# Performance work log

Measured on AMD Instinct MI355X. Metric: run time of the kernel, lower is better.

The kernel has to match this reference:

```python
import jax, jax.numpy as jnp
import numpy as np

B, S, D = 4, 2048, 768   # batch, seq_len, dim_inp
H, E = 12, 64            # num_heads, dim_out (per-head)
LN_EPS = 1e-5


def setup_inputs() -> dict:
    key = jax.random.key(0)
    ks = jax.random.split(key, 12)
    sd = 1.0 / np.sqrt(D)
    x = jax.random.normal(ks[0], (B, S, D), dtype=jnp.float32)
    Wq = jax.random.normal(ks[1], (H, D, E), dtype=jnp.float32) * sd
    bq = jax.random.normal(ks[2], (H, E), dtype=jnp.float32) * 0.02
    Wk = jax.random.normal(ks[3], (H, D, E), dtype=jnp.float32) * sd
    bk = jax.random.normal(ks[4], (H, E), dtype=jnp.float32) * 0.02
    Wv = jax.random.normal(ks[5], (H, D, E), dtype=jnp.float32) * sd
    bv = jax.random.normal(ks[6], (H, E), dtype=jnp.float32) * 0.02
    Wo = jax.random.normal(ks[7], (H * E, D), dtype=jnp.float32) * (1.0 / np.sqrt(H * E))
    bo = jax.random.normal(ks[8], (D,), dtype=jnp.float32) * 0.02
    gamma = jnp.ones((D,), dtype=jnp.float32)
    beta = jnp.zeros((D,), dtype=jnp.float32)
    return {"input_tensor": x, "Wq": Wq, "bq": bq, "Wk": Wk, "bk": bk,
            "Wv": Wv, "bv": bv, "Wo": Wo, "bo": bo, "gamma": gamma, "beta": beta}


def reference(input_tensor, Wq, bq, Wk, bk, Wv, bv, Wo, bo, gamma, beta):
    x = input_tensor  # [B,S,D]
    # all heads at once: [B,H,S,E]
    q = jnp.einsum('bsd,hde->bhse', x, Wq) + bq[None, :, None, :]
    k = jnp.einsum('bsd,hde->bhse', x, Wk) + bk[None, :, None, :]
    v = jnp.einsum('bsd,hde->bhse', x, Wv) + bv[None, :, None, :]
    # NOTE: original divides by sqrt(seq_len) (query.size(1)), not sqrt(head_dim)
    scale = jnp.sqrt(jnp.float32(q.shape[2]))
    scores = jnp.einsum('bhse,bhte->bhst', q, k) / scale  # [B,H,S,S]
    attn = jax.nn.softmax(scores, axis=-1)
    ctx = jnp.einsum('bhst,bhte->bhse', attn, v)          # [B,H,S,E]
    # concat heads along last dim: [B,S,H*E]
    ctx = ctx.transpose(0, 2, 1, 3).reshape(x.shape[0], x.shape[1], -1)
    proj = ctx @ Wo + bo                                   # [B,S,D]
    h = x + proj
    mu = jnp.mean(h, axis=-1, keepdims=True)
    var = jnp.mean(jnp.square(h - mu), axis=-1, keepdims=True)
    y = (h - mu) * jax.lax.rsqrt(var + LN_EPS) * gamma + beta
    return y
```

## Files before the change

### kernel.cpp

```cpp
#include <hip/hip_runtime.h>


typedef __bf16 bf16x8 __attribute__((ext_vector_type(8)));
typedef __bf16 bf16x4 __attribute__((ext_vector_type(4)));
typedef float  f32x4  __attribute__((ext_vector_type(4)));
typedef float  f32x16 __attribute__((ext_vector_type(16)));
typedef unsigned u32x4 __attribute__((ext_vector_type(4)));

#define MFMA16(a,b,c) __builtin_amdgcn_mfma_f32_16x16x32_bf16((a),(b),(c),0,0,0)
#define MFMA32(a,b,c) __builtin_amdgcn_mfma_f32_32x32x16_bf16((a),(b),(c),0,0,0)
#define QSCALE2 (0.022097086912079612f * 1.4426950408889634f)

__device__ __forceinline__ void gload16(const void* g, void* l) {
  __builtin_amdgcn_global_load_lds((const __attribute__((address_space(1))) void*)g,
                                   (__attribute__((address_space(3))) void*)l, 16, 0, 0);
}

__global__ __launch_bounds__(256) void pack_kernel(
    const float* __restrict__ x, const float* __restrict__ Wq,
    const float* __restrict__ Wk, const float* __restrict__ Wv,
    const float* __restrict__ Wo,
    __bf16* __restrict__ xb, __bf16* __restrict__ wqkv, __bf16* __restrict__ wot) {
  int tid = blockIdx.x * 256 + threadIdx.x;
  int nth = gridDim.x * 256;
  for (int i = tid; i < 8192 * 768 / 4; i += nth) {
    float4 v = ((const float4*)x)[i];
    bf16x4 o; o[0] = (__bf16)v.x; o[1] = (__bf16)v.y; o[2] = (__bf16)v.z; o[3] = (__bf16)v.w;
    ((bf16x4*)xb)[i] = o;
  }
  for (int i = tid; i < 3 * 768 * 768; i += nth) {
    int n = i / 768, d = i - n * 768;
    int p = n / 768;
    int wn = n - p * 768;
    int h = wn >> 6, e = wn & 63;
    const float* W = (p == 0) ? Wq : (p == 1) ? Wk : Wv;
    wqkv[i] = (__bf16)W[(h * 768 + d) * 64 + e];
  }
  for (int i = tid; i < 768 * 768; i += nth) {
    int n = i / 768, k = i - n * 768;
    wot[i] = (__bf16)Wo[k * 768 + n];
  }
}

#define GEMM_CORE(A_, Bt_, m0_, n0_)                                              \
  __shared__ __bf16 As[128 * 32];                                                 \
  __shared__ __bf16 Bs[128 * 32];                                                 \
  const int tid = threadIdx.x;                                                    \
  const int w = tid >> 6, lane = tid & 63, ln = lane & 15, hi = lane >> 4;        \
  const int wr = w >> 1, wc = w & 1;                                              \
  f32x4 acc[4][4];                                                                \
  {                                                                               \
    f32x4 z = {0.f, 0.f, 0.f, 0.f};                                               \
    _Pragma("unroll") for (int i = 0; i < 4; ++i)                                 \
      _Pragma("unroll") for (int j = 0; j < 4; ++j) acc[i][j] = z;                \
  }                                                                               \
  const int co = 8 * (hi ^ ((ln >> 1) & 3));    \
  {                                                                               \
    const int r0 = tid >> 2;                                                      \
    const int cc = ((tid & 3) * 8) ^ (((r0 >> 1) & 3) << 3);    \
    const __bf16* ga0 = A_ + (size_t)(m0_ + r0) * 768 + cc;                       \
    const __bf16* ga1 = A_ + (size_t)(m0_ + 64 + r0) * 768 + cc;                  \
    const __bf16* gb0 = Bt_ + (size_t)(n0_ + r0) * 768 + cc;                      \
    const __bf16* gb1 = Bt_ + (size_t)(n0_ + 64 + r0) * 768 + cc;                 \
    __bf16* la0 = &As[w * 512];                                                   \
    __bf16* la1 = &As[2048 + w * 512];                                            \
    __bf16* lb0 = &Bs[w * 512];                                                   \
    __bf16* lb1 = &Bs[2048 + w * 512];                                            \
    for (int kt = 0; kt < 24; ++kt) {                                             \
      const int kk = kt * 32;                                                     \
      gload16(ga0 + kk, la0);                                                     \
      gload16(ga1 + kk, la1);                                                     \
      gload16(gb0 + kk, lb0);                                                     \
      gload16(gb1 + kk, lb1);                                                     \
      __syncthreads();                                                            \
      bf16x8 af[4], bfv[4];                                                       \
      _Pragma("unroll") for (int mt = 0; mt < 4; ++mt)                            \
        af[mt] = *(const bf16x8*)&As[(wr * 64 + mt * 16 + ln) * 32 + co];         \
      _Pragma("unroll") for (int nt = 0; nt < 4; ++nt)                            \
        bfv[nt] = *(const bf16x8*)&Bs[(wc * 64 + nt * 16 + ln) * 32 + co];        \
      _Pragma("unroll") for (int mt = 0; mt < 4; ++mt)                            \
        _Pragma("unroll") for (int nt = 0; nt < 4; ++nt)                          \
          acc[mt][nt] = MFMA16(af[mt], bfv[nt], acc[mt][nt]);                     \
      __syncthreads();                                                            \
    }                                                                             \
  }

__global__ __launch_bounds__(256) void gemm_qkv(
    const __bf16* __restrict__ A, const __bf16* __restrict__ Bt,
    const float* __restrict__ bq, const float* __restrict__ bk,
    const float* __restrict__ bv,
    __bf16* __restrict__ qb, __bf16* __restrict__ kb, __bf16* __restrict__ vt) {
  const int lin = blockIdx.y * 18 + blockIdx.x;
  const int swzb = (lin & 7) * 144 + (lin >> 3);
  const int m0 = (swzb / 18) * 128, n0 = (swzb % 18) * 128;
  GEMM_CORE(A, Bt, m0, n0)
  const int p = n0 / 768;
  const float* bias = (p == 0) ? bq : (p == 1) ? bk : bv;
  const float sc = (p == 0) ? QSCALE2 : 1.0f;
#pragma unroll
  for (int nt = 0; nt < 4; ++nt) {
    int n = n0 + wc * 64 + nt * 16 + ln;
    int wn = n - p * 768;
    int h = wn >> 6, e = wn & 63;
    float bb = bias[wn];
#pragma unroll
    for (int mt = 0; mt < 4; ++mt) {
      int mrow = m0 + wr * 64 + mt * 16 + hi * 4;
      int b = mrow >> 11, s0 = mrow & 2047;
      if (p == 2) {
        bf16x4 pk;
#pragma unroll
        for (int r = 0; r < 4; ++r) pk[r] = (__bf16)(acc[mt][nt][r] + bb);
        *(bf16x4*)&vt[(((size_t)b * 12 + h) * 64 + e) * 2048 + s0] = pk;
      } else {
        __bf16* dst = (p == 0) ? qb : kb;
#pragma unroll
        for (int r = 0; r < 4; ++r)
          dst[(((size_t)b * 12 + h) * 2048 + s0 + r) * 64 + e] =
              (__bf16)((acc[mt][nt][r] + bb) * sc);
      }
    }
  }
}

__global__ __launch_bounds__(256) void gemm_proj(
    const __bf16* __restrict__ A, const __bf16* __restrict__ Bt,
    const float* __restrict__ bo, const float* __restrict__ xres,
    float* __restrict__ hout) {
  const int lin = blockIdx.y * 6 + blockIdx.x;
  const int swzb = (lin & 7) * 48 + (lin >> 3);
  const int m0 = (swzb / 6) * 128, n0 = (swzb % 6) * 128;
  GEMM_CORE(A, Bt, m0, n0)
#pragma unroll
  for (int nt = 0; nt < 4; ++nt) {
    int n = n0 + wc * 64 + nt * 16 + ln;
    float bb = bo[n];
#pragma unroll
    for (int mt = 0; mt < 4; ++mt) {
      int mrow = m0 + wr * 64 + mt * 16 + hi * 4;
#pragma unroll
      for (int r = 0; r < 4; ++r) {
        size_t idx = (size_t)(mrow + r) * 768 + n;
        hout[idx] = acc[mt][nt][r] + bb + xres[idx];
      }
    }
  }
}

__global__ __launch_bounds__(256, 3) void attn_kernel(
    const __bf16* __restrict__ qb, const __bf16* __restrict__ kb,
    const __bf16* __restrict__ vt, __bf16* __restrict__ ctx) {
  __shared__ __align__(16) char lds[32768];
  const int tid = threadIdx.x;
  const int w = tid >> 6, lane = tid & 63;
  const int l31 = lane & 31, h = lane >> 5;
  const int bh = blockIdx.x;
  const int q0 = blockIdx.y * 128 + w * 32;

  const int o0 = tid * 16, o1 = o0 + 4096;
  const int r0s = o0 >> 7, cb0 = o0 & 127;
  const int r1s = o1 >> 7, cb1 = o1 & 127;
  const char* kgb = (const char*)(kb + (size_t)bh * 2048 * 64);
  const char* vgb = (const char*)(vt + (size_t)bh * 64 * 2048);
  const char* ksrc0 = kgb + r0s * 128 + (cb0 ^ ((r0s & 7) << 4));
  const char* ksrc1 = kgb + r1s * 128 + (cb1 ^ ((r1s & 7) << 4));
  const char* vsrc0 = vgb + r0s * 4096 + (cb0 ^ ((r0s & 7) << 4));
  const char* vsrc1 = vgb + r1s * 4096 + (cb1 ^ ((r1s & 7) << 4));
  char* kl0 = lds + w * 1024;
  char* vl0 = lds + 16384 + w * 1024;

#define STAGE(t_, b_) do {                                   \
    gload16(ksrc0 + (size_t)(t_) * 8192, kl0 + (b_) * 8192); \
    gload16(ksrc1 + (size_t)(t_) * 8192, kl0 + (b_) * 8192 + 4096); \
    gload16(vsrc0 + (size_t)(t_) * 128,  vl0 + (b_) * 8192); \
    gload16(vsrc1 + (size_t)(t_) * 128,  vl0 + (b_) * 8192 + 4096); \
  } while (0)

  const __bf16* qp = qb + ((size_t)bh * 2048 + q0 + l31) * 64 + h * 8;
  bf16x8 qf[4];
#pragma unroll
  for (int s = 0; s < 4; ++s) qf[s] = *(const bf16x8*)(qp + 16 * s);

  const int swz = (l31 & 7) << 4;
  const int krd = l31 * 128 + ((h * 16) ^ swz);
  const int vrd = 16384 + l31 * 128 + ((h * 16) ^ swz);
  int ka_[8], va_[8];
#pragma unroll
  for (int kvt = 0; kvt < 2; ++kvt)
#pragma unroll
    for (int s = 0; s < 4; ++s) ka_[kvt * 4 + s] = (krd + kvt * 4096) ^ (s * 32);
#pragma unroll
  for (int ks = 0; ks < 4; ++ks)
#pragma unroll
    for (int et = 0; et < 2; ++et) va_[ks * 2 + et] = (vrd + et * 4096) ^ (ks * 32);

  f32x16 FZ;
#pragma unroll
  for (int r = 0; r < 16; ++r) FZ[r] = 0.f;
  bf16x8 onesf;
#pragma unroll
  for (int j = 0; j < 8; ++j) onesf[j] = (__bf16)1.0f;

  f32x16 lacc = FZ;
  f32x16 cacc[2];
  cacc[0] = FZ; cacc[1] = FZ;

  STAGE(0, 0);
  __syncthreads();

#define PKPAIR(dst_, i_)                                                       \
  {                                                                            \
    float pa_ = __builtin_amdgcn_exp2f(sa[2 * (i_)]);                          \
    float pb_ = __builtin_amdgcn_exp2f(sa[2 * (i_) + 1]);                      \
    asm("v_cvt_pk_bf16_f32 %0, %1, %2" : "=v"(dst_) : "v"(pa_), "v"(pb_));     \
  }

#define TILEBODY(B_, T_)                                                       \
  {                                                                            \
    if ((T_) < 31) STAGE((T_) + 1, (B_) ^ 1);                                  \
    bf16x8 kf[2][4], vf[4][2];                                                 \
    _Pragma("unroll") for (int kvt = 0; kvt < 2; ++kvt)                        \
      _Pragma("unroll") for (int s = 0; s < 4; ++s)                            \
        kf[kvt][s] = *(const bf16x8*)(lds + (B_) * 8192 + ka_[kvt * 4 + s]);   \
    _Pragma("unroll") for (int ks = 0; ks < 4; ++ks)                           \
      _Pragma("unroll") for (int et = 0; et < 2; ++et)                         \
        vf[ks][et] = *(const bf16x8*)(lds + (B_) * 8192 + va_[ks * 2 + et]);   \
    u32x4 pau[4];                                                              \
    _Pragma("unroll") for (int kvt = 0; kvt < 2; ++kvt) {                      \
      __builtin_amdgcn_s_setprio(1);                                           \
      f32x16 sa = MFMA32(kf[kvt][0], qf[0], FZ);                               \
      sa = MFMA32(kf[kvt][1], qf[1], sa);                                      \
      sa = MFMA32(kf[kvt][2], qf[2], sa);                                      \
      sa = MFMA32(kf[kvt][3], qf[3], sa);                                      \
      __builtin_amdgcn_s_setprio(0);                                           \
      unsigned c0, c1, c2, c3, c4, c5, c6, c7;                                 \
      PKPAIR(c0, 0) PKPAIR(c1, 1) PKPAIR(c2, 2) PKPAIR(c3, 3)                  \
      PKPAIR(c4, 4) PKPAIR(c5, 5) PKPAIR(c6, 6) PKPAIR(c7, 7)                  \
      asm("v_permlane32_swap_b32 %0, %1" : "+v"(c0), "+v"(c2));                \
      asm("v_permlane32_swap_b32 %0, %1" : "+v"(c1), "+v"(c3));                \
      asm("v_permlane32_swap_b32 %0, %1" : "+v"(c4), "+v"(c6));                \
      asm("v_permlane32_swap_b32 %0, %1" : "+v"(c5), "+v"(c7));                \
      pau[2 * kvt][0] = c0; pau[2 * kvt][1] = c1;                              \
      pau[2 * kvt][2] = c2; pau[2 * kvt][3] = c3;                              \
      pau[2 * kvt + 1][0] = c4; pau[2 * kvt + 1][1] = c5;                      \
      pau[2 * kvt + 1][2] = c6; pau[2 * kvt + 1][3] = c7;                      \
      lacc = MFMA32(__builtin_bit_cast(bf16x8, pau[2 * kvt]), onesf, lacc);    \
      lacc = MFMA32(__builtin_bit_cast(bf16x8, pau[2 * kvt + 1]), onesf, lacc);\
    }                                                                          \
    __builtin_amdgcn_s_setprio(1);                                             \
    _Pragma("unroll") for (int ks = 0; ks < 4; ++ks) {                         \
      bf16x8 paf = __builtin_bit_cast(bf16x8, pau[ks]);                        \
      cacc[0] = MFMA32(paf, vf[ks][0], cacc[0]);                               \
      cacc[1] = MFMA32(paf, vf[ks][1], cacc[1]);                               \
    }                                                                          \
    __builtin_amdgcn_s_setprio(0);                                             \
    __syncthreads();                                                           \
  }

  for (int t = 0; t < 32; t += 2) {
    TILEBODY(0, t)
    TILEBODY(1, t + 1)
  }
#undef TILEBODY
#undef PKPAIR
#undef STAGE

  const int b = bh / 12, hh = bh - b * 12;
#pragma unroll
  for (int r = 0; r < 16; ++r) {
    const int ql = (r & 3) + 8 * (r >> 2) + 4 * h;
    float rl = __builtin_amdgcn_rcpf(lacc[r]);
    size_t base = ((size_t)b * 2048 + q0 + ql) * 768 + hh * 64 + l31;
    ctx[base]      = (__bf16)(cacc[0][r] * rl);
    ctx[base + 32] = (__bf16)(cacc[1][r] * rl);
  }
}

__global__ __launch_bounds__(256) void ln_kernel(
    const float* __restrict__ hb, const float* __restrict__ gamma,
    const float* __restrict__ beta, float* __restrict__ out) {
  __shared__ float ssum[4], ssq[4];
  const int row = blockIdx.x, t = threadIdx.x;
  const float* hr = hb + (size_t)row * 768;
  float v0 = hr[t], v1 = hr[t + 256], v2 = hr[t + 512];
  float sum = v0 + v1 + v2;
  float sq = v0 * v0 + v1 * v1 + v2 * v2;
#pragma unroll
  for (int mask = 1; mask < 64; mask <<= 1) {
    sum += __shfl_xor(sum, mask, 64);
    sq += __shfl_xor(sq, mask, 64);
  }
  const int w = t >> 6;
  if ((t & 63) == 0) { ssum[w] = sum; ssq[w] = sq; }
  __syncthreads();
  float s1 = ssum[0] + ssum[1] + ssum[2] + ssum[3];
  float s2 = ssq[0] + ssq[1] + ssq[2] + ssq[3];
  float mu = s1 * (1.0f / 768.0f);
  float var = s2 * (1.0f / 768.0f) - mu * mu;
  float rs = rsqrtf(var + 1e-5f);
  float* orow = out + (size_t)row * 768;
  orow[t]       = (v0 - mu) * rs * gamma[t]       + beta[t];
  orow[t + 256] = (v1 - mu) * rs * gamma[t + 256] + beta[t + 256];
  orow[t + 512] = (v2 - mu) * rs * gamma[t + 512] + beta[t + 512];
}

extern "C" void kernel_launch(void* const* d_in, const int* in_sizes, int n_in,
                              void* d_out, int out_size, void* d_ws, size_t ws_size,
                              hipStream_t stream) {
  const float* x     = (const float*)d_in[0];
  const float* Wq    = (const float*)d_in[1];
  const float* bq    = (const float*)d_in[2];
  const float* Wk    = (const float*)d_in[3];
  const float* bk    = (const float*)d_in[4];
  const float* Wv    = (const float*)d_in[5];
  const float* bv    = (const float*)d_in[6];
  const float* Wo    = (const float*)d_in[7];
  const float* bo    = (const float*)d_in[8];
  const float* gamma = (const float*)d_in[9];
  const float* beta  = (const float*)d_in[10];
  float* out = (float*)d_out;

  char* ws = (char*)d_ws;
  __bf16* xb   = (__bf16*)(ws);
  __bf16* wqkv = (__bf16*)(ws + 12582912);
  __bf16* wot  = (__bf16*)(ws + 16121856);
  __bf16* qb   = (__bf16*)(ws + 17301504);
  __bf16* kb   = (__bf16*)(ws + 29884416);
  __bf16* vt   = (__bf16*)(ws + 42467328);
  __bf16* ctx  = (__bf16*)(ws + 55050240);
  float*  hb   = (float*)(ws + 67633152);

  pack_kernel<<<dim3(1024), dim3(256), 0, stream>>>(x, Wq, Wk, Wv, Wo, xb, wqkv, wot);
  gemm_qkv<<<dim3(18, 64), dim3(256), 0, stream>>>(xb, wqkv, bq, bk, bv, qb, kb, vt);
  attn_kernel<<<dim3(48, 16), dim3(256), 0, stream>>>(qb, kb, vt, ctx);
  gemm_proj<<<dim3(6, 64), dim3(256), 0, stream>>>(ctx, wot, bo, x, hb);
  ln_kernel<<<dim3(8192), dim3(256), 0, stream>>>(hb, gamma, beta, out);
}
```

Measured before the change: 165.4 us.

## Double-buffer GEMM shared-memory tiles to overlap global loads with MFMA

Converts the shared GEMM core to a two-stage LDS ping-pong. The next K-tile is issued via global_load_lds into the alternate buffer before the current tile's MFMAs run, and one barrier per step replaces the previous two. This is meant to hide global load latency behind compute, at the cost of doubling the LDS footprint per block. That larger footprint could reduce occupancy.

```diff
diff --git a/kernel.cpp b/kernel.cpp
--- a/kernel.cpp
+++ b/kernel.cpp
@@ -42,9 +42,31 @@
   }
 }
 
+#define GEMM_STEP(B_, T_)                                                         \
+  {                                                                               \
+    if ((T_) < 23) {                                                              \
+      const int kk_ = ((T_) + 1) * 32;                                            \
+      gload16(ga0 + kk_, lA + ((B_) ^ 1) * 8192);                                 \
+      gload16(ga1 + kk_, lA + ((B_) ^ 1) * 8192 + 4096);                          \
+      gload16(gb0 + kk_, lB + ((B_) ^ 1) * 8192);                                 \
+      gload16(gb1 + kk_, lB + ((B_) ^ 1) * 8192 + 4096);                          \
+    }                                                                             \
+    bf16x8 af[4], bfv[4];                                                         \
+    _Pragma("unroll") for (int mt = 0; mt < 4; ++mt)                              \
+      af[mt] = *(const bf16x8*)((char*)As + (B_) * 8192 +                         \
+                                (wr * 64 + mt * 16 + ln) * 64 + co * 2);          \
+    _Pragma("unroll") for (int nt = 0; nt < 4; ++nt)                              \
+      bfv[nt] = *(const bf16x8*)((char*)Bs + (B_) * 8192 +                        \
+                                 (wc * 64 + nt * 16 + ln) * 64 + co * 2);         \
+    _Pragma("unroll") for (int mt = 0; mt < 4; ++mt)                              \
+      _Pragma("unroll") for (int nt = 0; nt < 4; ++nt)                            \
+        acc[mt][nt] = MFMA16(af[mt], bfv[nt], acc[mt][nt]);                       \
+    __syncthreads();                                                              \
+  }
+
 #define GEMM_CORE(A_, Bt_, m0_, n0_)                                              \
-  __shared__ __bf16 As[128 * 32];                                                 \
-  __shared__ __bf16 Bs[128 * 32];                                                 \
+  __shared__ __align__(16) __bf16 As[2][128 * 32];                                \
+  __shared__ __align__(16) __bf16 Bs[2][128 * 32];                                \
   const int tid = threadIdx.x;                                                    \
   const int w = tid >> 6, lane = tid & 63, ln = lane & 15, hi = lane >> 4;        \
   const int wr = w >> 1, wc = w & 1;                                              \
@@ -62,26 +84,14 @@
     const __bf16* ga1 = A_ + (size_t)(m0_ + 64 + r0) * 768 + cc;                  \
     const __bf16* gb0 = Bt_ + (size_t)(n0_ + r0) * 768 + cc;                      \
     const __bf16* gb1 = Bt_ + (size_t)(n0_ + 64 + r0) * 768 + cc;                 \
-    __bf16* la0 = &As[w * 512];                                                   \
-    __bf16* la1 = &As[2048 + w * 512];                                            \
-    __bf16* lb0 = &Bs[w * 512];                                                   \
-    __bf16* lb1 = &Bs[2048 + w * 512];                                            \
-    for (int kt = 0; kt < 24; ++kt) {                                             \
-      const int kk = kt * 32;                                                     \
-      gload16(ga0 + kk, la0);                                                     \
-      gload16(ga1 + kk, la1);                                                     \
-      gload16(gb0 + kk, lb0);                                                     \
-      gload16(gb1 + kk, lb1);                                                     \
-      __syncthreads();                                                            \
-      bf16x8 af[4], bfv[4];                                                       \
-      _Pragma("unroll") for (int mt = 0; mt < 4; ++mt)                            \
-        af[mt] = *(const bf16x8*)&As[(wr * 64 + mt * 16 + ln) * 32 + co];         \
-      _Pragma("unroll") for (int nt = 0; nt < 4; ++nt)                            \
-        bfv[nt] = *(const bf16x8*)&Bs[(wc * 64 + nt * 16 + ln) * 32 + co];        \
-      _Pragma("unroll") for (int mt = 0; mt < 4; ++mt)                            \
-        _Pragma("unroll") for (int nt = 0; nt < 4; ++nt)                          \
-          acc[mt][nt] = MFMA16(af[mt], bfv[nt], acc[mt][nt]);                     \
-      __syncthreads();                                                            \
+    char* lA = (char*)As + w * 1024;    \
+    char* lB = (char*)Bs + w * 1024;                                              \
+    gload16(ga0, lA);        gload16(ga1, lA + 4096);                             \
+    gload16(gb0, lB);        gload16(gb1, lB + 4096);                             \
+    __syncthreads();                                                              \
+    for (int kt = 0; kt < 24; kt += 2) {                                          \
+      GEMM_STEP(0, kt)                                                            \
+      GEMM_STEP(1, kt + 1)                                                        \
     }                                                                             \
   }
 
```

After: 166.8 us. About the same (+0.9%).
